# Performance work log

Measured on AMD Instinct MI355X. Metric: run time of the kernel, lower is better.

Reference implementation:

```python
import jax, jax.numpy as jnp
import numpy as np

N_NODES = 100000
N_EDGES = 1600000


def gcn_conv(x, src, dst, W, b, n_nodes):
    # GCNConv: linear transform, then symmetrically-normalized scatter-add
    # (self-loops already appended to src/dst by caller)
    h = x @ W  # [N, out]
    ones = jnp.ones(src.shape[0], dtype=x.dtype)
    deg = jax.ops.segment_sum(ones, dst, num_segments=n_nodes)  # in-degree incl. self-loop
    dinv = jnp.where(deg > 0, jax.lax.rsqrt(deg), jnp.zeros_like(deg))
    norm = dinv[src] * dinv[dst]  # [E]
    out = jax.ops.segment_sum(norm[:, None] * h[src], dst, num_segments=n_nodes)
    return out + b


def setup_inputs() -> dict:
    key = jax.random.key(0)
    ks = jax.random.split(key, 8)
    in_ch, nhid, out_ch = 128, 48, 32
    x = jax.random.normal(ks[0], (N_NODES, in_ch), dtype=jnp.float32)
    edge_index = jax.random.randint(ks[1], (2, N_EDGES), 0, N_NODES, dtype=jnp.int64)
    s1 = 1.0 / np.sqrt(in_ch)
    s2 = 1.0 / np.sqrt(nhid)
    W1 = jax.random.uniform(ks[2], (in_ch, nhid), jnp.float32, -s1, s1)
    b1 = jnp.zeros((nhid,), jnp.float32)
    Wmu = jax.random.uniform(ks[3], (nhid, out_ch), jnp.float32, -s2, s2)
    bmu = jnp.zeros((out_ch,), jnp.float32)
    Wls = jax.random.uniform(ks[4], (nhid, out_ch), jnp.float32, -s2, s2)
    bls = jnp.zeros((out_ch,), jnp.float32)
    return {"x": x, "edge_index": edge_index, "W1": W1, "b1": b1,
            "Wmu": Wmu, "bmu": bmu, "Wls": Wls, "bls": bls}


def reference(x, edge_index, W1, b1, Wmu, bmu, Wls, bls):
    n = x.shape[0]
    loop = jnp.arange(n, dtype=edge_index.dtype)
    src = jnp.concatenate([edge_index[0], loop])
    dst = jnp.concatenate([edge_index[1], loop])
    h = jax.nn.relu(gcn_conv(x, src, dst, W1, b1, n))
    mu = gcn_conv(h, src, dst, Wmu, bmu, n)
    logstd = gcn_conv(h, src, dst, Wls, bls, n)
    return mu, logstd
```

## Files before the change

kernel.cpp:

```cpp
#include <hip/hip_runtime.h>
#include <hip/hip_fp16.h>

#define NN 100000
#define NE 1600000
#define FIN 128
#define FH 48
#define FO 32

#define LB 7
#define BKT_NODES 128
#define NBKT ((NN + BKT_NODES - 1) / BKT_NODES)
#define PBLK 250
#define EPB (NE / PBLK)
#define EPB4 (EPB / 4)
#define P2CAP 4096

#define GNPB 42
#define GCAP 1024

__device__ inline float2 h2f2(unsigned int u) {
  __half2 h = __builtin_bit_cast(__half2, u);
  return __half22float2(h);
}
__device__ inline unsigned int f2h2(float a, float b) {
  __half2 h = __floats2half2_rn(a, b);
  return __builtin_bit_cast(unsigned int, h);
}


__global__ __launch_bounds__(256) void p1_hist(const int4* __restrict__ dst4, int* __restrict__ H) {
  __shared__ int hist[NBKT];
  const int t = threadIdx.x, blk = blockIdx.x;
  for (int i = t; i < NBKT; i += 256) hist[i] = 0;
  __syncthreads();
  const int k0 = blk * EPB4;
  for (int k = t; k < EPB4; k += 256) {
    int4 d = dst4[k0 + k];
    atomicAdd(&hist[d.x >> LB], 1);
    atomicAdd(&hist[d.y >> LB], 1);
    atomicAdd(&hist[d.z >> LB], 1);
    atomicAdd(&hist[d.w >> LB], 1);
  }
  __syncthreads();
  for (int i = t; i < NBKT; i += 256) H[blk * NBKT + i] = hist[i];
}

__global__ __launch_bounds__(256) void p1_colscan(int* __restrict__ H, int* __restrict__ tot) {
  int b = blockIdx.x * 256 + threadIdx.x;
  if (b >= NBKT) return;
  int run = 0;
  for (int xcd = 0; xcd < 8; ++xcd) {
    for (int blk = xcd; blk < PBLK; blk += 8) {
      int v = H[blk * NBKT + b];
      H[blk * NBKT + b] = run;
      run += v;
    }
  }
  tot[b] = run;
}

__global__ __launch_bounds__(256) void p1_scan(const int* __restrict__ tot, int* __restrict__ base,
                                               int* __restrict__ off) {
  __shared__ int s[256];
  const int t = threadIdx.x;
  int c[4]; int sum = 0;
  #pragma unroll
  for (int k = 0; k < 4; ++k) {
    int idx = 4 * t + k;
    c[k] = (idx < NBKT) ? tot[idx] : 0;
    sum += c[k];
  }
  s[t] = sum;
  __syncthreads();
  for (int o = 1; o < 256; o <<= 1) {
    int v = (t >= o) ? s[t - o] : 0;
    __syncthreads();
    s[t] += v;
    __syncthreads();
  }
  int run = s[t] - sum;
  #pragma unroll
  for (int k = 0; k < 4; ++k) {
    int idx = 4 * t + k;
    if (idx < NBKT) base[idx] = run;
    run += c[k];
  }
  if (t == 255) { base[NBKT] = run; off[NN] = run; }
}

__global__ __launch_bounds__(256) void p1_scatter(const int4* __restrict__ src4, const int4* __restrict__ dst4,
                                                  const int* __restrict__ H, const int* __restrict__ base,
                                                  int* __restrict__ pairs) {
  __shared__ int cur[NBKT];
  const int t = threadIdx.x, blk = blockIdx.x;
  for (int i = t; i < NBKT; i += 256) cur[i] = base[i] + H[blk * NBKT + i];
  __syncthreads();
  const int k0 = blk * EPB4;
  for (int k = t; k < EPB4; k += 256) {
    int4 s = src4[k0 + k];
    int4 d = dst4[k0 + k];
    int b0 = d.x >> LB, b1 = d.y >> LB, b2 = d.z >> LB, b3 = d.w >> LB;
    int p0 = atomicAdd(&cur[b0], 1);
    pairs[p0] = s.x | ((d.x & (BKT_NODES - 1)) << 17);
    int p1 = atomicAdd(&cur[b1], 1);
    pairs[p1] = s.y | ((d.y & (BKT_NODES - 1)) << 17);
    int p2 = atomicAdd(&cur[b2], 1);
    pairs[p2] = s.z | ((d.z & (BKT_NODES - 1)) << 17);
    int p3 = atomicAdd(&cur[b3], 1);
    pairs[p3] = s.w | ((d.w & (BKT_NODES - 1)) << 17);
  }
}

__global__ __launch_bounds__(256) void p2_bucket(const int* __restrict__ pairs, const int* __restrict__ base,
                                                 int* __restrict__ csr, int* __restrict__ off,
                                                 float* __restrict__ dinv) {
  __shared__ int stage[P2CAP];
  __shared__ int cnt[BKT_NODES];
  __shared__ int s[BKT_NODES];
  const int t = threadIdx.x, b = blockIdx.x;
  const int j0 = base[b], j1 = base[b + 1];
  const int ne = j1 - j0;
  const bool fits = (ne <= P2CAP);

  if (t < BKT_NODES) cnt[t] = 0;
  if (fits) {
    for (int j = t; j < ne; j += 256) stage[j] = pairs[j0 + j];
  }
  __syncthreads();
  if (fits) {
    for (int j = t; j < ne; j += 256) atomicAdd(&cnt[stage[j] >> 17], 1);
  } else {
    for (int j = j0 + t; j < j1; j += 256) atomicAdd(&cnt[pairs[j] >> 17], 1);
  }
  __syncthreads();
  int myc = 0;
  if (t < BKT_NODES) { myc = cnt[t]; s[t] = myc; }
  __syncthreads();
  for (int o = 1; o < BKT_NODES; o <<= 1) {
    int v = (t >= o && t < BKT_NODES) ? s[t - o] : 0;
    __syncthreads();
    if (t < BKT_NODES) s[t] += v;
    __syncthreads();
  }
  int loc = 0;
  if (t < BKT_NODES) loc = s[t] - myc;
  const int n = b * BKT_NODES + t;
  if (t < BKT_NODES && n < NN) {
    off[n] = j0 + loc;
    dinv[n] = rsqrtf((float)myc + 1.0f);
  }
  __syncthreads();
  if (t < BKT_NODES) s[t] = loc;
  __syncthreads();
  if (fits) {
    for (int j = t; j < ne; j += 256) {
      int p = stage[j];
      int pos = atomicAdd(&s[p >> 17], 1);
      csr[j0 + pos] = p & 0x1FFFF;
    }
  } else {
    for (int j = j0 + t; j < j1; j += 256) {
      int p = pairs[j];
      int pos = atomicAdd(&s[p >> 17], 1);
      csr[j0 + pos] = p & 0x1FFFF;
    }
  }
}


__global__ __launch_bounds__(256) void k_gemm1(const float* __restrict__ x, const float* __restrict__ W1,
                                               __half* __restrict__ t1h) {
  __shared__ float xs[64][132];
  __shared__ float ws[FIN][FH];
  const int t = threadIdx.x;
  const int row0 = blockIdx.x * 64;

  for (int i = t; i < FIN * FH; i += 256) ws[i / FH][i % FH] = W1[i];
  for (int i = t; i < 64 * (FIN / 4); i += 256) {
    int r = i >> 5, c4 = i & 31;
    float4 v = make_float4(0.f, 0.f, 0.f, 0.f);
    if (row0 + r < NN) v = ((const float4*)x)[(size_t)(row0 + r) * (FIN / 4) + c4];
    xs[r][c4 * 4 + 0] = v.x; xs[r][c4 * 4 + 1] = v.y;
    xs[r][c4 * 4 + 2] = v.z; xs[r][c4 * 4 + 3] = v.w;
  }
  __syncthreads();

  const int row = t >> 2;
  const int cg  = (t & 3) * 12;
  float acc[12];
  #pragma unroll
  for (int j = 0; j < 12; ++j) acc[j] = 0.f;

  #pragma unroll 4
  for (int k = 0; k < FIN; ++k) {
    float xv = xs[row][k];
    const float4* wp = (const float4*)&ws[k][cg];
    float4 w0 = wp[0], w1 = wp[1], w2 = wp[2];
    acc[0] += xv * w0.x; acc[1] += xv * w0.y; acc[2]  += xv * w0.z; acc[3]  += xv * w0.w;
    acc[4] += xv * w1.x; acc[5] += xv * w1.y; acc[6]  += xv * w1.z; acc[7]  += xv * w1.w;
    acc[8] += xv * w2.x; acc[9] += xv * w2.y; acc[10] += xv * w2.z; acc[11] += xv * w2.w;
  }

  const int grow = row0 + row;
  if (grow < NN) {
    uint2* p = (uint2*)(t1h + (size_t)grow * FH + cg);
    p[0] = make_uint2(f2h2(acc[0], acc[1]), f2h2(acc[2],  acc[3]));
    p[1] = make_uint2(f2h2(acc[4], acc[5]), f2h2(acc[6],  acc[7]));
    p[2] = make_uint2(f2h2(acc[8], acc[9]), f2h2(acc[10], acc[11]));
  }
}


#define GATHER_BODY(FEAT, SS, DS, A)                                             \
  {                                                                              \
    int j = jb;                                                                  \
    for (; j + 4 <= je; j += 4) {                                                \
      int s0 = SS[j], s1 = SS[j + 1], s2 = SS[j + 2], s3 = SS[j + 3];            \
      float nv0 = DS[j] * di, nv1 = DS[j + 1] * di;                              \
      float nv2 = DS[j + 2] * di, nv3 = DS[j + 3] * di;                          \
      uint4 r0 = FEAT[(size_t)s0 * 6 + f8];                                      \
      uint4 r1 = FEAT[(size_t)s1 * 6 + f8];                                      \
      uint4 r2 = FEAT[(size_t)s2 * 6 + f8];                                      \
      uint4 r3 = FEAT[(size_t)s3 * 6 + f8];                                      \
      float2 q0, q1, q2, q3;                                                     \
      q0 = h2f2(r0.x); q1 = h2f2(r0.y); q2 = h2f2(r0.z); q3 = h2f2(r0.w);        \
      A[0] += nv0 * q0.x; A[1] += nv0 * q0.y; A[2] += nv0 * q1.x;                \
      A[3] += nv0 * q1.y; A[4] += nv0 * q2.x; A[5] += nv0 * q2.y;                \
      A[6] += nv0 * q3.x; A[7] += nv0 * q3.y;                                    \
      q0 = h2f2(r1.x); q1 = h2f2(r1.y); q2 = h2f2(r1.z); q3 = h2f2(r1.w);        \
      A[0] += nv1 * q0.x; A[1] += nv1 * q0.y; A[2] += nv1 * q1.x;                \
      A[3] += nv1 * q1.y; A[4] += nv1 * q2.x; A[5] += nv1 * q2.y;                \
      A[6] += nv1 * q3.x; A[7] += nv1 * q3.y;                                    \
      q0 = h2f2(r2.x); q1 = h2f2(r2.y); q2 = h2f2(r2.z); q3 = h2f2(r2.w);        \
      A[0] += nv2 * q0.x; A[1] += nv2 * q0.y; A[2] += nv2 * q1.x;                \
      A[3] += nv2 * q1.y; A[4] += nv2 * q2.x; A[5] += nv2 * q2.y;                \
      A[6] += nv2 * q3.x; A[7] += nv2 * q3.y;                                    \
      q0 = h2f2(r3.x); q1 = h2f2(r3.y); q2 = h2f2(r3.z); q3 = h2f2(r3.w);        \
      A[0] += nv3 * q0.x; A[1] += nv3 * q0.y; A[2] += nv3 * q1.x;                \
      A[3] += nv3 * q1.y; A[4] += nv3 * q2.x; A[5] += nv3 * q2.y;                \
      A[6] += nv3 * q3.x; A[7] += nv3 * q3.y;                                    \
    }                                                                            \
    for (; j < je; ++j) {                                                        \
      int s = SS[j];                                                             \
      float nv = DS[j] * di;                                                     \
      uint4 r = FEAT[(size_t)s * 6 + f8];                                        \
      float2 q0 = h2f2(r.x), q1 = h2f2(r.y), q2 = h2f2(r.z), q3 = h2f2(r.w);     \
      A[0] += nv * q0.x; A[1] += nv * q0.y; A[2] += nv * q1.x;                   \
      A[3] += nv * q1.y; A[4] += nv * q2.x; A[5] += nv * q2.y;                   \
      A[6] += nv * q3.x; A[7] += nv * q3.y;                                      \
    }                                                                            \
  }


__global__ __launch_bounds__(256) void k_gather1(const int* __restrict__ off, const int* __restrict__ csr,
                                                 const __half* __restrict__ feat16, const float* __restrict__ dinv,
                                                 const float* __restrict__ bias, __half* __restrict__ out16) {
  __shared__ int   sstage[GCAP];
  __shared__ float dstage[GCAP];
  const int t = threadIdx.x;
  const int n0 = blockIdx.x * GNPB;
  const int nend = (n0 + GNPB < NN) ? n0 + GNPB : NN;
  const int e0 = off[n0];
  const int ec = off[nend] - e0;
  const bool fits = (ec <= GCAP);
  if (fits) {
    for (int j = t; j < ec; j += 256) {
      int s = csr[e0 + j];
      sstage[j] = s;
      dstage[j] = dinv[s];
    }
  }
  __syncthreads();

  const int local = t / 6;
  const int f8 = t - local * 6;
  const int node = n0 + local;
  if (local >= GNPB || node >= NN) return;

  const uint4* feat = (const uint4*)feat16;
  const float di = dinv[node];
  const float sn = di * di;
  uint4 rs = feat[(size_t)node * 6 + f8];
  float a[8];
  {
    float2 q0 = h2f2(rs.x), q1 = h2f2(rs.y), q2 = h2f2(rs.z), q3 = h2f2(rs.w);
    a[0] = q0.x * sn; a[1] = q0.y * sn; a[2] = q1.x * sn; a[3] = q1.y * sn;
    a[4] = q2.x * sn; a[5] = q2.y * sn; a[6] = q3.x * sn; a[7] = q3.y * sn;
  }

  if (fits) {
    const int jb = off[node] - e0;
    const int je = off[node + 1] - e0;
    GATHER_BODY(feat, sstage, dstage, a)
  } else {
    const int jb = off[node];
    const int je = off[node + 1];
    for (int j = jb; j < je; ++j) {
      int s = csr[j];
      float nv = dinv[s] * di;
      uint4 r = feat[(size_t)s * 6 + f8];
      float2 q0 = h2f2(r.x), q1 = h2f2(r.y), q2 = h2f2(r.z), q3 = h2f2(r.w);
      a[0] += nv * q0.x; a[1] += nv * q0.y; a[2] += nv * q1.x; a[3] += nv * q1.y;
      a[4] += nv * q2.x; a[5] += nv * q2.y; a[6] += nv * q3.x; a[7] += nv * q3.y;
    }
  }

  const float4* b4 = (const float4*)(bias + f8 * 8);
  float4 bb0 = b4[0], bb1 = b4[1];
  a[0] = fmaxf(a[0] + bb0.x, 0.f); a[1] = fmaxf(a[1] + bb0.y, 0.f);
  a[2] = fmaxf(a[2] + bb0.z, 0.f); a[3] = fmaxf(a[3] + bb0.w, 0.f);
  a[4] = fmaxf(a[4] + bb1.x, 0.f); a[5] = fmaxf(a[5] + bb1.y, 0.f);
  a[6] = fmaxf(a[6] + bb1.z, 0.f); a[7] = fmaxf(a[7] + bb1.w, 0.f);
  uint4 o;
  o.x = f2h2(a[0], a[1]); o.y = f2h2(a[2], a[3]);
  o.z = f2h2(a[4], a[5]); o.w = f2h2(a[6], a[7]);
  ((uint4*)out16)[(size_t)node * 6 + f8] = o;
}


__global__ __launch_bounds__(256) void k_gather_gemm2(const int* __restrict__ off, const int* __restrict__ csr,
                                                      const __half* __restrict__ feat16, const float* __restrict__ dinv,
                                                      const float* __restrict__ Wmu, const float* __restrict__ bmu,
                                                      const float* __restrict__ Wls, const float* __restrict__ bls,
                                                      float* __restrict__ out) {
  __shared__ int   sstage[GCAP];
  __shared__ float dstage[GCAP];
  __shared__ float wall[FH][2 * FO];
  __shared__ float as2[GNPB][FH + 1];
  const int t = threadIdx.x;
  const int n0 = blockIdx.x * GNPB;
  const int nend = (n0 + GNPB < NN) ? n0 + GNPB : NN;
  const int e0 = off[n0];
  const int ec = off[nend] - e0;
  const bool fits = (ec <= GCAP);

  for (int i = t; i < FH * 2 * FO; i += 256) {
    int k = i >> 6, c = i & 63;
    wall[k][c] = (c < FO) ? Wmu[k * FO + c] : Wls[k * FO + (c - FO)];
  }
  if (fits) {
    for (int j = t; j < ec; j += 256) {
      int s = csr[e0 + j];
      sstage[j] = s;
      dstage[j] = dinv[s];
    }
  }
  __syncthreads();

  const int local = t / 6;
  const int f8 = t - local * 6;
  const int node = n0 + local;
  const bool active = (local < GNPB) && (node < NN);

  if (active) {
    const uint4* feat = (const uint4*)feat16;
    const float di = dinv[node];
    const float sn = di * di;
    uint4 rs = feat[(size_t)node * 6 + f8];
    float a[8];
    {
      float2 q0 = h2f2(rs.x), q1 = h2f2(rs.y), q2 = h2f2(rs.z), q3 = h2f2(rs.w);
      a[0] = q0.x * sn; a[1] = q0.y * sn; a[2] = q1.x * sn; a[3] = q1.y * sn;
      a[4] = q2.x * sn; a[5] = q2.y * sn; a[6] = q3.x * sn; a[7] = q3.y * sn;
    }
    if (fits) {
      const int jb = off[node] - e0;
      const int je = off[node + 1] - e0;
      GATHER_BODY(feat, sstage, dstage, a)
    } else {
      const int jb = off[node];
      const int je = off[node + 1];
      for (int j = jb; j < je; ++j) {
        int s = csr[j];
        float nv = dinv[s] * di;
        uint4 r = feat[(size_t)s * 6 + f8];
        float2 q0 = h2f2(r.x), q1 = h2f2(r.y), q2 = h2f2(r.z), q3 = h2f2(r.w);
        a[0] += nv * q0.x; a[1] += nv * q0.y; a[2] += nv * q1.x; a[3] += nv * q1.y;
        a[4] += nv * q2.x; a[5] += nv * q2.y; a[6] += nv * q3.x; a[7] += nv * q3.y;
      }
    }
    float* ap = &as2[local][f8 * 8];
    ap[0] = a[0]; ap[1] = a[1]; ap[2] = a[2]; ap[3] = a[3];
    ap[4] = a[4]; ap[5] = a[5]; ap[6] = a[6]; ap[7] = a[7];
  }
  __syncthreads();

  for (int o = t; o < GNPB * 2 * FO; o += 256) {
    const int ln = o >> 6;
    const int c = o & 63;
    const int grow = n0 + ln;
    if (grow < NN) {
      float acc = (c < FO) ? bmu[c] : bls[c - FO];
      #pragma unroll
      for (int k = 0; k < FH; ++k) acc += as2[ln][k] * wall[k][c];
      if (c < FO) out[(size_t)grow * FO + c] = acc;
      else        out[(size_t)NN * FO + (size_t)grow * FO + (c - FO)] = acc;
    }
  }
}


extern "C" void kernel_launch(void* const* d_in, const int* in_sizes, int n_in,
                              void* d_out, int out_size, void* d_ws, size_t ws_size,
                              hipStream_t stream) {
  const float* x   = (const float*)d_in[0];
  const int*   ei  = (const int*)d_in[1];
  const float* W1  = (const float*)d_in[2];
  const float* b1  = (const float*)d_in[3];
  const float* Wmu = (const float*)d_in[4];
  const float* bmu = (const float*)d_in[5];
  const float* Wls = (const float*)d_in[6];
  const float* bls = (const float*)d_in[7];
  float* out = (float*)d_out;

  const int4* src4 = (const int4*)ei;
  const int4* dst4 = (const int4*)(ei + NE);

  char* base_p = (char*)d_ws;
  int*    pairs = (int*)base_p;
  int*    csr   = pairs + (size_t)NE;
  __half* t1h   = (__half*)(csr + (size_t)NE);
  __half* h16   = t1h + (size_t)NN * FH;
  int*    H     = (int*)(h16 + (size_t)NN * FH);
  int*    tot   = H + (size_t)PBLK * NBKT;
  int*    bkb   = tot + NBKT;
  int*    off   = bkb + NBKT + 1;
  float*  dinv  = (float*)(off + NN + 1);

  p1_hist   <<<PBLK, 256, 0, stream>>>(dst4, H);
  p1_colscan<<<(NBKT + 255) / 256, 256, 0, stream>>>(H, tot);
  p1_scan   <<<1, 256, 0, stream>>>(tot, bkb, off);
  p1_scatter<<<PBLK, 256, 0, stream>>>(src4, dst4, H, bkb, pairs);
  p2_bucket <<<NBKT, 256, 0, stream>>>(pairs, bkb, csr, off, dinv);

  k_gemm1<<<(NN + 63) / 64, 256, 0, stream>>>(x, W1, t1h);
  k_gather1<<<(NN + GNPB - 1) / GNPB, 256, 0, stream>>>(off, csr, t1h, dinv, b1, h16);

  k_gather_gemm2<<<(NN + GNPB - 1) / GNPB, 256, 0, stream>>>(
      off, csr, h16, dinv, Wmu, bmu, Wls, bls, out);
}
```

Baseline: 292.7 us.

## Fold symmetric normalization into source features to drop per-edge dinv gathers

Pre-scales GEMM1 output rows by the source node's dinv and scales the layer-1 output by dinv again after ReLU. The gathers then become plain unweighted sums followed by one final multiply by the destination dinv. This removes the per-edge random dinv lookups, the dstage shared buffer and the per-edge multiplies, and it unrolls the gather by 8 for more memory-level parallelism. Pre-scaled values stored in fp16 may shift rounding slightly, and the fallback path now uses the unrolled macro directly on global csr.

Measured after the change: 274.5 us. 6.2% less time.

```diff
diff --git a/kernel.cpp b/kernel.cpp
--- a/kernel.cpp
+++ b/kernel.cpp
@@ -169,7 +169,7 @@
 
 
 __global__ __launch_bounds__(256) void k_gemm1(const float* __restrict__ x, const float* __restrict__ W1,
-                                               __half* __restrict__ t1h) {
+                                               const float* __restrict__ dinv, __half* __restrict__ t1h) {
   __shared__ float xs[64][132];
   __shared__ float ws[FIN][FH];
   const int t = threadIdx.x;
@@ -203,6 +203,9 @@
 
   const int grow = row0 + row;
   if (grow < NN) {
+    const float dv = dinv[grow];
+    #pragma unroll
+    for (int j = 0; j < 12; ++j) acc[j] *= dv;
     uint2* p = (uint2*)(t1h + (size_t)grow * FH + cg);
     p[0] = make_uint2(f2h2(acc[0], acc[1]), f2h2(acc[2],  acc[3]));
     p[1] = make_uint2(f2h2(acc[4], acc[5]), f2h2(acc[6],  acc[7]));
@@ -211,43 +214,39 @@
 }
 
 
-#define GATHER_BODY(FEAT, SS, DS, A)                                             \
+#define ACC8(R)                                                                  \
+  { float2 q0 = h2f2(R.x), q1 = h2f2(R.y), q2 = h2f2(R.z), q3 = h2f2(R.w);       \
+    a[0] += q0.x; a[1] += q0.y; a[2] += q1.x; a[3] += q1.y;                      \
+    a[4] += q2.x; a[5] += q2.y; a[6] += q3.x; a[7] += q3.y; }
+
+#define GATHER_SUM(FEAT, SS)                                                     \
   {                                                                              \
     int j = jb;                                                                  \
-    for (; j + 4 <= je; j += 4) {                                                \
-      int s0 = SS[j], s1 = SS[j + 1], s2 = SS[j + 2], s3 = SS[j + 3];            \
-      float nv0 = DS[j] * di, nv1 = DS[j + 1] * di;                              \
-      float nv2 = DS[j + 2] * di, nv3 = DS[j + 3] * di;                          \
+    for (; j + 8 <= je; j += 8) {                                                \
+      int s0 = SS[j],     s1 = SS[j + 1], s2 = SS[j + 2], s3 = SS[j + 3];        \
+      int s4 = SS[j + 4], s5 = SS[j + 5], s6 = SS[j + 6], s7 = SS[j + 7];        \
       uint4 r0 = FEAT[(size_t)s0 * 6 + f8];                                      \
       uint4 r1 = FEAT[(size_t)s1 * 6 + f8];                                      \
       uint4 r2 = FEAT[(size_t)s2 * 6 + f8];                                      \
       uint4 r3 = FEAT[(size_t)s3 * 6 + f8];                                      \
-      float2 q0, q1, q2, q3;                                                     \
-      q0 = h2f2(r0.x); q1 = h2f2(r0.y); q2 = h2f2(r0.z); q3 = h2f2(r0.w);        \
-      A[0] += nv0 * q0.x; A[1] += nv0 * q0.y; A[2] += nv0 * q1.x;                \
-      A[3] += nv0 * q1.y; A[4] += nv0 * q2.x; A[5] += nv0 * q2.y;                \
-      A[6] += nv0 * q3.x; A[7] += nv0 * q3.y;                                    \
-      q0 = h2f2(r1.x); q1 = h2f2(r1.y); q2 = h2f2(r1.z); q3 = h2f2(r1.w);        \
-      A[0] += nv1 * q0.x; A[1] += nv1 * q0.y; A[2] += nv1 * q1.x;                \
-      A[3] += nv1 * q1.y; A[4] += nv1 * q2.x; A[5] += nv1 * q2.y;                \
-      A[6] += nv1 * q3.x; A[7] += nv1 * q3.y;                                    \
-      q0 = h2f2(r2.x); q1 = h2f2(r2.y); q2 = h2f2(r2.z); q3 = h2f2(r2.w);        \
-      A[0] += nv2 * q0.x; A[1] += nv2 * q0.y; A[2] += nv2 * q1.x;                \
-      A[3] += nv2 * q1.y; A[4] += nv2 * q2.x; A[5] += nv2 * q2.y;                \
-      A[6] += nv2 * q3.x; A[7] += nv2 * q3.y;                                    \
-      q0 = h2f2(r3.x); q1 = h2f2(r3.y); q2 = h2f2(r3.z); q3 = h2f2(r3.w);        \
-      A[0] += nv3 * q0.x; A[1] += nv3 * q0.y; A[2] += nv3 * q1.x;                \
-      A[3] += nv3 * q1.y; A[4] += nv3 * q2.x; A[5] += nv3 * q2.y;                \
-      A[6] += nv3 * q3.x; A[7] += nv3 * q3.y;                                    \
+      uint4 r4 = FEAT[(size_t)s4 * 6 + f8];                                      \
+      uint4 r5 = FEAT[(size_t)s5 * 6 + f8];                                      \
+      uint4 r6 = FEAT[(size_t)s6 * 6 + f8];                                      \
+      uint4 r7 = FEAT[(size_t)s7 * 6 + f8];                                      \
+      ACC8(r0) ACC8(r1) ACC8(r2) ACC8(r3) ACC8(r4) ACC8(r5) ACC8(r6) ACC8(r7)    \
+    }                                                                            \
+    for (; j + 4 <= je; j += 4) {                                                \
+      int s0 = SS[j], s1 = SS[j + 1], s2 = SS[j + 2], s3 = SS[j + 3];            \
+      uint4 r0 = FEAT[(size_t)s0 * 6 + f8];                                      \
+      uint4 r1 = FEAT[(size_t)s1 * 6 + f8];                                      \
+      uint4 r2 = FEAT[(size_t)s2 * 6 + f8];                                      \
+      uint4 r3 = FEAT[(size_t)s3 * 6 + f8];                                      \
+      ACC8(r0) ACC8(r1) ACC8(r2) ACC8(r3)                                        \
     }                                                                            \
     for (; j < je; ++j) {                                                        \
       int s = SS[j];                                                             \
-      float nv = DS[j] * di;                                                     \
       uint4 r = FEAT[(size_t)s * 6 + f8];                                        \
-      float2 q0 = h2f2(r.x), q1 = h2f2(r.y), q2 = h2f2(r.z), q3 = h2f2(r.w);     \
-      A[0] += nv * q0.x; A[1] += nv * q0.y; A[2] += nv * q1.x;                   \
-      A[3] += nv * q1.y; A[4] += nv * q2.x; A[5] += nv * q2.y;                   \
-      A[6] += nv * q3.x; A[7] += nv * q3.y;                                      \
+      ACC8(r)                                                                    \
     }                                                                            \
   }
 
@@ -255,8 +254,7 @@
 __global__ __launch_bounds__(256) void k_gather1(const int* __restrict__ off, const int* __restrict__ csr,
                                                  const __half* __restrict__ feat16, const float* __restrict__ dinv,
                                                  const float* __restrict__ bias, __half* __restrict__ out16) {
-  __shared__ int   sstage[GCAP];
-  __shared__ float dstage[GCAP];
+  __shared__ int sstage[GCAP];
   const int t = threadIdx.x;
   const int n0 = blockIdx.x * GNPB;
   const int nend = (n0 + GNPB < NN) ? n0 + GNPB : NN;
@@ -264,11 +262,7 @@
   const int ec = off[nend] - e0;
   const bool fits = (ec <= GCAP);
   if (fits) {
-    for (int j = t; j < ec; j += 256) {
-      int s = csr[e0 + j];
-      sstage[j] = s;
-      dstage[j] = dinv[s];
-    }
+    for (int j = t; j < ec; j += 256) sstage[j] = csr[e0 + j];
   }
   __syncthreads();
 
@@ -279,38 +273,30 @@
 
   const uint4* feat = (const uint4*)feat16;
   const float di = dinv[node];
-  const float sn = di * di;
   uint4 rs = feat[(size_t)node * 6 + f8];
   float a[8];
   {
     float2 q0 = h2f2(rs.x), q1 = h2f2(rs.y), q2 = h2f2(rs.z), q3 = h2f2(rs.w);
-    a[0] = q0.x * sn; a[1] = q0.y * sn; a[2] = q1.x * sn; a[3] = q1.y * sn;
-    a[4] = q2.x * sn; a[5] = q2.y * sn; a[6] = q3.x * sn; a[7] = q3.y * sn;
+    a[0] = q0.x; a[1] = q0.y; a[2] = q1.x; a[3] = q1.y;
+    a[4] = q2.x; a[5] = q2.y; a[6] = q3.x; a[7] = q3.y;
   }
 
   if (fits) {
     const int jb = off[node] - e0;
     const int je = off[node + 1] - e0;
-    GATHER_BODY(feat, sstage, dstage, a)
+    GATHER_SUM(feat, sstage)
   } else {
     const int jb = off[node];
     const int je = off[node + 1];
-    for (int j = jb; j < je; ++j) {
-      int s = csr[j];
-      float nv = dinv[s] * di;
-      uint4 r = feat[(size_t)s * 6 + f8];
-      float2 q0 = h2f2(r.x), q1 = h2f2(r.y), q2 = h2f2(r.z), q3 = h2f2(r.w);
-      a[0] += nv * q0.x; a[1] += nv * q0.y; a[2] += nv * q1.x; a[3] += nv * q1.y;
-      a[4] += nv * q2.x; a[5] += nv * q2.y; a[6] += nv * q3.x; a[7] += nv * q3.y;
-    }
+    GATHER_SUM(feat, csr)
   }
 
   const float4* b4 = (const float4*)(bias + f8 * 8);
   float4 bb0 = b4[0], bb1 = b4[1];
-  a[0] = fmaxf(a[0] + bb0.x, 0.f); a[1] = fmaxf(a[1] + bb0.y, 0.f);
-  a[2] = fmaxf(a[2] + bb0.z, 0.f); a[3] = fmaxf(a[3] + bb0.w, 0.f);
-  a[4] = fmaxf(a[4] + bb1.x, 0.f); a[5] = fmaxf(a[5] + bb1.y, 0.f);
-  a[6] = fmaxf(a[6] + bb1.z, 0.f); a[7] = fmaxf(a[7] + bb1.w, 0.f);
+  a[0] = di * fmaxf(di * a[0] + bb0.x, 0.f); a[1] = di * fmaxf(di * a[1] + bb0.y, 0.f);
+  a[2] = di * fmaxf(di * a[2] + bb0.z, 0.f); a[3] = di * fmaxf(di * a[3] + bb0.w, 0.f);
+  a[4] = di * fmaxf(di * a[4] + bb1.x, 0.f); a[5] = di * fmaxf(di * a[5] + bb1.y, 0.f);
+  a[6] = di * fmaxf(di * a[6] + bb1.z, 0.f); a[7] = di * fmaxf(di * a[7] + bb1.w, 0.f);
   uint4 o;
   o.x = f2h2(a[0], a[1]); o.y = f2h2(a[2], a[3]);
   o.z = f2h2(a[4], a[5]); o.w = f2h2(a[6], a[7]);
@@ -324,9 +310,8 @@
                                                       const float* __restrict__ Wls, const float* __restrict__ bls,
                                                       float* __restrict__ out) {
   __shared__ int   sstage[GCAP];
-  __shared__ float dstage[GCAP];
   __shared__ float wall[FH][2 * FO];
-  __shared__ float as2[GNPB][FH + 1];
+  __shared__ float as2[GNPB][FH + 4];
   const int t = threadIdx.x;
   const int n0 = blockIdx.x * GNPB;
   const int nend = (n0 + GNPB < NN) ? n0 + GNPB : NN;
@@ -339,11 +324,7 @@
     wall[k][c] = (c < FO) ? Wmu[k * FO + c] : Wls[k * FO + (c - FO)];
   }
   if (fits) {
-    for (int j = t; j < ec; j += 256) {
-      int s = csr[e0 + j];
-      sstage[j] = s;
-      dstage[j] = dinv[s];
-    }
+    for (int j = t; j < ec; j += 256) sstage[j] = csr[e0 + j];
   }
   __syncthreads();
 
@@ -355,33 +336,25 @@
   if (active) {
     const uint4* feat = (const uint4*)feat16;
     const float di = dinv[node];
-    const float sn = di * di;
     uint4 rs = feat[(size_t)node * 6 + f8];
     float a[8];
     {
       float2 q0 = h2f2(rs.x), q1 = h2f2(rs.y), q2 = h2f2(rs.z), q3 = h2f2(rs.w);
-      a[0] = q0.x * sn; a[1] = q0.y * sn; a[2] = q1.x * sn; a[3] = q1.y * sn;
-      a[4] = q2.x * sn; a[5] = q2.y * sn; a[6] = q3.x * sn; a[7] = q3.y * sn;
+      a[0] = q0.x; a[1] = q0.y; a[2] = q1.x; a[3] = q1.y;
+      a[4] = q2.x; a[5] = q2.y; a[6] = q3.x; a[7] = q3.y;
     }
     if (fits) {
       const int jb = off[node] - e0;
       const int je = off[node + 1] - e0;
-      GATHER_BODY(feat, sstage, dstage, a)
+      GATHER_SUM(feat, sstage)
     } else {
       const int jb = off[node];
       const int je = off[node + 1];
-      for (int j = jb; j < je; ++j) {
-        int s = csr[j];
-        float nv = dinv[s] * di;
-        uint4 r = feat[(size_t)s * 6 + f8];
-        float2 q0 = h2f2(r.x), q1 = h2f2(r.y), q2 = h2f2(r.z), q3 = h2f2(r.w);
-        a[0] += nv * q0.x; a[1] += nv * q0.y; a[2] += nv * q1.x; a[3] += nv * q1.y;
-        a[4] += nv * q2.x; a[5] += nv * q2.y; a[6] += nv * q3.x; a[7] += nv * q3.y;
-      }
+      GATHER_SUM(feat, csr)
     }
     float* ap = &as2[local][f8 * 8];
-    ap[0] = a[0]; ap[1] = a[1]; ap[2] = a[2]; ap[3] = a[3];
-    ap[4] = a[4]; ap[5] = a[5]; ap[6] = a[6]; ap[7] = a[7];
+    ap[0] = di * a[0]; ap[1] = di * a[1]; ap[2] = di * a[2]; ap[3] = di * a[3];
+    ap[4] = di * a[4]; ap[5] = di * a[5]; ap[6] = di * a[6]; ap[7] = di * a[7];
   }
   __syncthreads();
 
@@ -433,7 +406,7 @@
   p1_scatter<<<PBLK, 256, 0, stream>>>(src4, dst4, H, bkb, pairs);
   p2_bucket <<<NBKT, 256, 0, stream>>>(pairs, bkb, csr, off, dinv);
 
-  k_gemm1<<<(NN + 63) / 64, 256, 0, stream>>>(x, W1, t1h);
+  k_gemm1<<<(NN + 63) / 64, 256, 0, stream>>>(x, W1, dinv, t1h);
   k_gather1<<<(NN + GNPB - 1) / GNPB, 256, 0, stream>>>(off, csr, t1h, dinv, b1, h16);
 
   k_gather_gemm2<<<(NN + GNPB - 1) / GNPB, 256, 0, stream>>>(
```
